# Performance work log

Hardware: AMD Instinct MI355X
Metric: run time of the kernel (lower is better)

## Reference

```python
import jax, jax.numpy as jnp
import numpy as np

B, HW, C = 32, 56, 128
WS, SS, NH = 7, 3, 4
HD = C // NH
SCALE = HD ** -0.5
NWIN = (HW // WS) ** 2  # 64 windows per image
N = WS * WS             # 49 tokens per window


def _build_constants():
    # relative position index [N, N] into flattened (13*13) bias table
    coords = np.stack(np.meshgrid(np.arange(WS), np.arange(WS), indexing='ij'))  # [2,7,7]
    cf = coords.reshape(2, -1)                       # [2,49]
    rel = cf[:, :, None] - cf[:, None, :]            # [2,49,49]
    rel = rel.transpose(1, 2, 0).copy()              # [49,49,2]
    rel[:, :, 0] += WS - 1
    rel[:, :, 1] += WS - 1
    rel[:, :, 0] *= 2 * WS - 1
    pos_index = rel.sum(-1)                          # [49,49]
    # shifted-window attention mask [nW, N, N]
    img = np.zeros((HW, HW))
    sl = (slice(0, -WS), slice(-WS, -SS), slice(-SS, None))
    cnt = 0
    for h in sl:
        for w in sl:
            img[h, w] = cnt
            cnt += 1
    mw = img.reshape(HW // WS, WS, HW // WS, WS).transpose(0, 2, 1, 3).reshape(NWIN, N)
    am = mw[:, None, :] - mw[:, :, None]             # unsqueeze(1) - unsqueeze(2)
    am = np.where(am != 0, -100.0, 0.0).astype(np.float32)
    return jnp.asarray(pos_index), jnp.asarray(am)

POS_INDEX, ATTN_MASK = _build_constants()


def _ln(x, w, b, eps=1e-5):
    mu = x.mean(-1, keepdims=True)
    var = ((x - mu) ** 2).mean(-1, keepdims=True)
    return (x - mu) * jax.lax.rsqrt(var + eps) * w + b


def setup_inputs() -> dict:
    key = jax.random.key(0)
    ks = jax.random.split(key, 10)
    s = 0.02
    return {
        'x': jax.random.normal(ks[0], (B, HW * HW, C), jnp.float32),
        'norm1_w': jnp.ones((C,), jnp.float32),
        'norm1_b': jnp.zeros((C,), jnp.float32),
        'qkv_w': jax.random.normal(ks[1], (C, 3 * C), jnp.float32) * s,
        'qkv_b': jax.random.normal(ks[2], (3 * C,), jnp.float32) * s,
        'proj_w': jax.random.normal(ks[3], (C, C), jnp.float32) * s,
        'proj_b': jax.random.normal(ks[4], (C,), jnp.float32) * s,
        'pos_bias_table': jax.random.normal(ks[5], (2 * WS - 1, 2 * WS - 1, NH), jnp.float32) * s,
        'mlp_w1': jax.random.normal(ks[6], (C, 4 * C), jnp.float32) * s,
        'mlp_b1': jnp.zeros((4 * C,), jnp.float32),
        'mlp_w2': jax.random.normal(ks[7], (4 * C, C), jnp.float32) * s,
        'mlp_b2': jnp.zeros((C,), jnp.float32),
        'norm2_w': jnp.ones((C,), jnp.float32),
        'norm2_b': jnp.zeros((C,), jnp.float32),
    }


def reference(x, norm1_w, norm1_b, qkv_w, qkv_b, proj_w, proj_b, pos_bias_table,
              mlp_w1, mlp_b1, mlp_w2, mlp_b2, norm2_w, norm2_b):
    G = HW // WS  # grid of windows per side
    Bw = B * NWIN
    shortcut = x
    y = _ln(x, norm1_w, norm1_b).reshape(B, HW, HW, C)
    # cyclic shift
    y = jnp.roll(y, (-SS, -SS), axis=(1, 2))
    # window partition -> [B*nW, 49, C]
    yw = y.reshape(B, G, WS, G, WS, C).transpose(0, 1, 3, 2, 4, 5).reshape(Bw, N, C)
    # qkv projection
    qkv = (yw @ qkv_w + qkv_b).reshape(Bw, N, 3, NH, HD).transpose(2, 0, 3, 1, 4)
    q, k, v = qkv[0] * SCALE, qkv[1], qkv[2]  # [Bw, NH, N, HD]
    attn = jnp.einsum('bhnd,bhmd->bhnm', q, k)
    # relative position bias [NH, N, N]
    bias = pos_bias_table.reshape(-1, NH)[POS_INDEX]  # [N,N,NH]
    attn = attn + bias.transpose(2, 0, 1)[None]
    # shift mask per window
    attn = attn.reshape(B, NWIN, NH, N, N) + ATTN_MASK[None, :, None]
    attn = jax.nn.softmax(attn.reshape(Bw, NH, N, N), axis=-1)
    out = jnp.einsum('bhnm,bhmd->bhnd', attn, v).transpose(0, 2, 1, 3).reshape(Bw, N, C)
    out = out @ proj_w + proj_b
    # window reverse
    out = out.reshape(B, G, G, WS, WS, C).transpose(0, 1, 3, 2, 4, 5).reshape(B, HW, HW, C)
    out = jnp.roll(out, (SS, SS), axis=(1, 2)).reshape(B, HW * HW, C)
    x = shortcut + out
    h = _ln(x, norm2_w, norm2_b)
    h = jax.nn.gelu(h @ mlp_w1 + mlp_b1, approximate=False) @ mlp_w2 + mlp_b2
    return x + h
```

## Files before the change

kernel.cpp:

```cpp
#include <hip/hip_runtime.h>
#include <hip/hip_bf16.h>

#define NTOK 100352
#define SCALE_Q 0.17677669529663687f

typedef __bf16 bf16x8 __attribute__((ext_vector_type(8)));
typedef float f32x4 __attribute__((ext_vector_type(4)));
struct bf2 { __hip_bfloat16 x, y; };

__device__ __forceinline__ int wt_to_tok(int wt) {
  int w = wt / 49, n = wt - w * 49;
  int b = w >> 6, wi = w & 63;
  int gh = wi >> 3, gw = wi & 7;
  int r = n / 7, c = n - r * 7;
  int hs = gh * 7 + r + 3; if (hs >= 56) hs -= 56;
  int ws = gw * 7 + c + 3; if (ws >= 56) ws -= 56;
  return (b * 56 + hs) * 56 + ws;
}

__global__ __launch_bounds__(256) void prep_all(const float* __restrict__ qkvw,
                                                const float* __restrict__ projw,
                                                const float* __restrict__ w1,
                                                const float* __restrict__ w2,
                                                __hip_bfloat16* __restrict__ dst) {
  int i = blockIdx.x * 256 + threadIdx.x;
  float v;
  if (i < 49152) { int n = i >> 7, k = i & 127; v = qkvw[k * 384 + n]; }
  else if (i < 65536) { int j = i - 49152; int n = j >> 7, k = j & 127; v = projw[k * 128 + n]; }
  else if (i < 131072) { int j = i - 65536; int n = j >> 7, k = j & 127; v = w1[k * 512 + n]; }
  else { int j = i - 131072; int n = j / 512, k = j - n * 512; v = w2[k * 128 + n]; }
  dst[i] = __float2bfloat16(v);
}

__global__ __launch_bounds__(256) void ln1_apply(const float* __restrict__ x,
                                                 const float* __restrict__ nw,
                                                 const float* __restrict__ nb,
                                                 __hip_bfloat16* __restrict__ xn) {
  int wt = blockIdx.x * 4 + (threadIdx.x >> 6);
  int lane = threadIdx.x & 63;
  int tok = wt_to_tok(wt);
  float2 v = *(const float2*)(x + (size_t)tok * 128 + lane * 2);
  float s = v.x + v.y, ss = v.x * v.x + v.y * v.y;
#pragma unroll
  for (int off = 32; off; off >>= 1) {
    s += __shfl_xor(s, off);
    ss += __shfl_xor(ss, off);
  }
  float mu = s * (1.0f / 128.0f);
  float rstd = rsqrtf(ss * (1.0f / 128.0f) - mu * mu + 1e-5f);
  float2 wv = *(const float2*)(nw + lane * 2);
  float2 bv = *(const float2*)(nb + lane * 2);
  bf2 o;
  o.x = __float2bfloat16((v.x - mu) * rstd * wv.x + bv.x);
  o.y = __float2bfloat16((v.y - mu) * rstd * wv.y + bv.y);
  *(bf2*)(xn + (size_t)wt * 128 + lane * 2) = o;
}

__global__ __launch_bounds__(256) void attn_mfma(const __hip_bfloat16* __restrict__ qkv,
                                                 const float* __restrict__ ptab,
                                                 __hip_bfloat16* __restrict__ attnout) {
  __shared__ __align__(16) char lds[4 * 12288];
  const int tid = threadIdx.x;
  const int lane = tid & 63, h = tid >> 6;
  const int w = blockIdx.x;
  const int wi = w & 63, gh = wi >> 3, gw = wi & 7;
  char* Pl = lds + h * 12288;
  char* VTl = Pl + 8192;
  const int lxi = lane & 15, lq = lane >> 4, lg4 = (lane >> 4) * 4;

  const __hip_bfloat16* base = qkv + (size_t)w * 49 * 384 + h * 32;
  __hip_bfloat16* op = attnout + (size_t)w * 49 * 128 + h * 32;

  bf16x8 qa[4], kb[4];
#pragma unroll
  for (int mi = 0; mi < 4; ++mi) {
    int t = mi * 16 + lxi; if (t > 48) t = 48;
    qa[mi] = *(const bf16x8*)(base + (size_t)t * 384 + lq * 8);
    kb[mi] = *(const bf16x8*)(base + (size_t)t * 384 + 128 + lq * 8);
  }
  {
    union { bf16x8 v; __hip_bfloat16 e[8]; } vv[4];
    const __hip_bfloat16* vp = base + (size_t)(lane < 49 ? lane : 0) * 384 + 256;
#pragma unroll
    for (int q = 0; q < 4; ++q) vv[q].v = *(const bf16x8*)(vp + q * 8);
    __hip_bfloat16 z = __float2bfloat16(0.0f);
#pragma unroll
    for (int q = 0; q < 4; ++q)
#pragma unroll
      for (int e = 0; e < 8; ++e) {
        int d = q * 8 + e;
        __hip_bfloat16 val = (lane < 49) ? vv[q].e[e] : z;
        *(__hip_bfloat16*)(VTl + d * 128 + ((lane * 2) ^ ((d & 7) << 4))) = val;
      }
  }

  f32x4 s[4][4] = {};
#pragma unroll
  for (int mi = 0; mi < 4; ++mi)
#pragma unroll
    for (int ni = 0; ni < 4; ++ni)
      s[mi][ni] = __builtin_amdgcn_mfma_f32_16x16x32_bf16(qa[mi], kb[ni], s[mi][ni], 0, 0, 0);

  int rj[4], cj[4], cntj[4], jbad[4];
#pragma unroll
  for (int ni = 0; ni < 4; ++ni) {
    int jc = ni * 16 + lxi;
    jbad[ni] = (jc > 48);
    int jj = jbad[ni] ? 48 : jc;
    rj[ni] = jj / 7; cj[ni] = jj - rj[ni] * 7;
    int hj = gh * 7 + rj[ni], wj = gw * 7 + cj[ni];
    cntj[ni] = (hj < 49 ? 0 : (hj < 53 ? 3 : 6)) + (wj < 49 ? 0 : (wj < 53 ? 1 : 2));
  }
#pragma unroll
  for (int mi = 0; mi < 4; ++mi)
#pragma unroll
    for (int j = 0; j < 4; ++j) {
      int i = mi * 16 + lg4 + j; if (i > 48) i = 48;
      int ri = i / 7, ci = i - ri * 7;
      int hi_ = gh * 7 + ri, wi_ = gw * 7 + ci;
      int cnti = (hi_ < 49 ? 0 : (hi_ < 53 ? 3 : 6)) + (wi_ < 49 ? 0 : (wi_ < 53 ? 1 : 2));
#pragma unroll
      for (int ni = 0; ni < 4; ++ni) {
        float b = ptab[((ri - rj[ni] + 6) * 13 + (ci - cj[ni] + 6)) * 4 + h];
        float val = s[mi][ni][j] * SCALE_Q + b;
        if (cnti != cntj[ni]) val -= 100.0f;
        if (jbad[ni]) val = -1e30f;
        s[mi][ni][j] = val;
      }
    }

#pragma unroll
  for (int mi = 0; mi < 4; ++mi)
#pragma unroll
    for (int j = 0; j < 4; ++j) {
      float m = fmaxf(fmaxf(s[mi][0][j], s[mi][1][j]), fmaxf(s[mi][2][j], s[mi][3][j]));
#pragma unroll
      for (int off = 8; off; off >>= 1) m = fmaxf(m, __shfl_xor(m, off));
      float e[4], sum = 0.0f;
#pragma unroll
      for (int ni = 0; ni < 4; ++ni) { e[ni] = __expf(s[mi][ni][j] - m); sum += e[ni]; }
#pragma unroll
      for (int off = 8; off; off >>= 1) sum += __shfl_xor(sum, off);
      float inv = 1.0f / sum;
#pragma unroll
      for (int ni = 0; ni < 4; ++ni) s[mi][ni][j] = e[ni] * inv;
    }

#pragma unroll
  for (int mi = 0; mi < 4; ++mi)
#pragma unroll
    for (int j = 0; j < 4; ++j) {
      int row = mi * 16 + lg4 + j;
      int sw = (row & 7) << 4;
      char* prow = Pl + row * 128;
#pragma unroll
      for (int ni = 0; ni < 4; ++ni)
        *(__hip_bfloat16*)(prow + (((ni * 16 + lxi) * 2) ^ sw)) =
            __float2bfloat16(s[mi][ni][j]);
    }

  __syncthreads();

  f32x4 o[4][2] = {};
#pragma unroll
  for (int ks = 0; ks < 2; ++ks) {
    bf16x8 pa[4], vb[2];
#pragma unroll
    for (int mi = 0; mi < 4; ++mi) {
      int row = mi * 16 + lxi;
      pa[mi] = *(const bf16x8*)(Pl + row * 128 + ((ks * 64 + lq * 16) ^ ((row & 7) << 4)));
    }
#pragma unroll
    for (int ni = 0; ni < 2; ++ni) {
      int row = ni * 16 + lxi;
      vb[ni] = *(const bf16x8*)(VTl + row * 128 + ((ks * 64 + lq * 16) ^ ((row & 7) << 4)));
    }
#pragma unroll
    for (int mi = 0; mi < 4; ++mi)
#pragma unroll
      for (int ni = 0; ni < 2; ++ni)
        o[mi][ni] = __builtin_amdgcn_mfma_f32_16x16x32_bf16(pa[mi], vb[ni], o[mi][ni], 0, 0, 0);
  }

#pragma unroll
  for (int mi = 0; mi < 4; ++mi)
#pragma unroll
    for (int j = 0; j < 4; ++j) {
      int q = mi * 16 + lg4 + j;
      if (q < 49) {
#pragma unroll
        for (int ni = 0; ni < 2; ++ni)
          op[(size_t)q * 128 + ni * 16 + lxi] = __float2bfloat16(o[mi][ni][j]);
      }
    }
}

template<int EPI>
__global__ __launch_bounds__(256) void gemm_mfma(
    const __hip_bfloat16* __restrict__ A, int lda,
    const __hip_bfloat16* __restrict__ Wt,
    const float* __restrict__ bias,
    void* __restrict__ outv, int ldo,
    __hip_bfloat16* __restrict__ out2,
    const float* __restrict__ nw, const float* __restrict__ nb,
    const float* __restrict__ res, int K)
{
  __shared__ __align__(16) char AsB[128 * 256];
  __shared__ __align__(16) char BsB[128 * 256];
  const int tid = threadIdx.x;
  const int m0 = blockIdx.x * 128, n0 = blockIdx.y * 128;
  const int srow = tid >> 1;
  const int scol = (tid & 1) * 64;
  const int lane = tid & 63, wid = tid >> 6;
  const int wm = wid >> 1, wn = wid & 1;
  const int lrow = lane & 15, lq = lane >> 4;

  f32x4 acc[4][4] = {};

  for (int k0 = 0; k0 < K; k0 += 128) {
    {
      const char* ap = (const char*)A + ((size_t)(m0 + srow) * lda + k0 + scol) * 2;
      char* dst = AsB + srow * 256;
      int sw = (srow & 7) << 4;
#pragma unroll
      for (int t = 0; t < 8; ++t) {
        int4 raw = *(const int4*)(ap + t * 16);
        *(int4*)(dst + ((scol * 2 + t * 16) ^ sw)) = raw;
      }
    }
    {
      const char* bp = (const char*)Wt + ((size_t)(n0 + srow) * K + k0 + scol) * 2;
      char* dst = BsB + srow * 256;
      int sw = (srow & 7) << 4;
#pragma unroll
      for (int t = 0; t < 8; ++t) {
        int4 raw = *(const int4*)(bp + t * 16);
        *(int4*)(dst + ((scol * 2 + t * 16) ^ sw)) = raw;
      }
    }
    __syncthreads();
#pragma unroll
    for (int ks = 0; ks < 4; ++ks) {
      int kb = ks * 64 + lq * 16;
      bf16x8 af[4], bfr[4];
#pragma unroll
      for (int mi = 0; mi < 4; ++mi) {
        int r = wm * 64 + mi * 16 + lrow;
        af[mi] = *(const bf16x8*)(AsB + r * 256 + (kb ^ ((r & 7) << 4)));
      }
#pragma unroll
      for (int ni = 0; ni < 4; ++ni) {
        int r = wn * 64 + ni * 16 + lrow;
        bfr[ni] = *(const bf16x8*)(BsB + r * 256 + (kb ^ ((r & 7) << 4)));
      }
#pragma unroll
      for (int mi = 0; mi < 4; ++mi)
#pragma unroll
        for (int ni = 0; ni < 4; ++ni)
          acc[mi][ni] = __builtin_amdgcn_mfma_f32_16x16x32_bf16(af[mi], bfr[ni], acc[mi][ni], 0, 0, 0);
    }
    __syncthreads();
  }

  float bv[4];
#pragma unroll
  for (int ni = 0; ni < 4; ++ni) bv[ni] = bias[n0 + wn * 64 + ni * 16 + lrow];

  if (EPI == 4) {
    float* x2 = (float*)outv;
    float* redS = (float*)AsB;
    float* redQ = (float*)(AsB + 1024);
    float nwc[4], nbc[4];
#pragma unroll
    for (int ni = 0; ni < 4; ++ni) {
      int colg = wn * 64 + ni * 16 + lrow;
      nwc[ni] = nw[colg]; nbc[ni] = nb[colg];
    }
    int toks[4][4];
#pragma unroll
    for (int mi = 0; mi < 4; ++mi)
#pragma unroll
      for (int j = 0; j < 4; ++j) {
        int row = wm * 64 + mi * 16 + lq * 4 + j;
        int tok = wt_to_tok(m0 + row);
        toks[mi][j] = tok;
        float s = 0.0f, ss = 0.0f;
#pragma unroll
        for (int ni = 0; ni < 4; ++ni) {
          int colg = wn * 64 + ni * 16 + lrow;
          float val = acc[mi][ni][j] + bv[ni] + res[(size_t)tok * 128 + colg];
          x2[(size_t)tok * 128 + colg] = val;
          acc[mi][ni][j] = val;
          s += val; ss += val * val;
        }
#pragma unroll
        for (int off = 8; off; off >>= 1) {
          s += __shfl_xor(s, off);
          ss += __shfl_xor(ss, off);
        }
        if (lrow == 0) { redS[row * 2 + wn] = s; redQ[row * 2 + wn] = ss; }
      }
    __syncthreads();
#pragma unroll
    for (int mi = 0; mi < 4; ++mi)
#pragma unroll
      for (int j = 0; j < 4; ++j) {
        int row = wm * 64 + mi * 16 + lq * 4 + j;
        float s = redS[row * 2] + redS[row * 2 + 1];
        float ss = redQ[row * 2] + redQ[row * 2 + 1];
        float mu = s * (1.0f / 128.0f);
        float rstd = rsqrtf(ss * (1.0f / 128.0f) - mu * mu + 1e-5f);
        int tok = toks[mi][j];
#pragma unroll
        for (int ni = 0; ni < 4; ++ni) {
          int colg = wn * 64 + ni * 16 + lrow;
          float xnv = (acc[mi][ni][j] - mu) * rstd * nwc[ni] + nbc[ni];
          out2[(size_t)tok * 128 + colg] = __float2bfloat16(xnv);
        }
      }
    return;
  }

#pragma unroll
  for (int mi = 0; mi < 4; ++mi) {
#pragma unroll
    for (int j = 0; j < 4; ++j) {
      int rowg = m0 + wm * 64 + mi * 16 + lq * 4 + j;
#pragma unroll
      for (int ni = 0; ni < 4; ++ni) {
        int colg = n0 + wn * 64 + ni * 16 + lrow;
        float val = acc[mi][ni][j] + bv[ni];
        if (EPI == 0) {
          ((__hip_bfloat16*)outv)[(size_t)rowg * ldo + colg] = __float2bfloat16(val);
        } else if (EPI == 1) {
          float g = 0.5f * val * (1.0f + erff(val * 0.70710678118654752f));
          ((__hip_bfloat16*)outv)[(size_t)rowg * ldo + colg] = __float2bfloat16(g);
        } else {
          float r = res[(size_t)rowg * 128 + colg];
          ((float*)outv)[(size_t)rowg * 128 + colg] = val + r;
        }
      }
    }
  }
}

extern "C" void kernel_launch(void* const* d_in, const int* in_sizes, int n_in,
                              void* d_out, int out_size, void* d_ws, size_t ws_size,
                              hipStream_t stream) {
  (void)in_sizes; (void)n_in; (void)out_size; (void)ws_size;
  const float* x     = (const float*)d_in[0];
  const float* n1w   = (const float*)d_in[1];
  const float* n1b   = (const float*)d_in[2];
  const float* qkvw  = (const float*)d_in[3];
  const float* qkvb  = (const float*)d_in[4];
  const float* projw = (const float*)d_in[5];
  const float* projb = (const float*)d_in[6];
  const float* ptab  = (const float*)d_in[7];
  const float* w1    = (const float*)d_in[8];
  const float* b1    = (const float*)d_in[9];
  const float* w2    = (const float*)d_in[10];
  const float* b2    = (const float*)d_in[11];
  const float* n2w   = (const float*)d_in[12];
  const float* n2b   = (const float*)d_in[13];
  float* out = (float*)d_out;

  char* ws = (char*)d_ws;
  __hip_bfloat16* xn      = (__hip_bfloat16*)ws;
  __hip_bfloat16* qkv     = (__hip_bfloat16*)(ws + 25690112);
  __hip_bfloat16* attnout = (__hip_bfloat16*)(ws + 102760448);
  __hip_bfloat16* u       = (__hip_bfloat16*)(ws + 25690112);
  float* x2               = (float*)(ws + 128450560);
  __hip_bfloat16* x2n     = (__hip_bfloat16*)(ws + 179830784);
  __hip_bfloat16* wbase   = (__hip_bfloat16*)(ws + 205520896);
  __hip_bfloat16* qkvwT  = wbase;
  __hip_bfloat16* projwT = wbase + 49152;
  __hip_bfloat16* w1T    = wbase + 65536;
  __hip_bfloat16* w2T    = wbase + 131072;

  prep_all<<<768, 256, 0, stream>>>(qkvw, projw, w1, w2, wbase);
  ln1_apply<<<NTOK / 4, 256, 0, stream>>>(x, n1w, n1b, xn);
  gemm_mfma<0><<<dim3(784, 3), 256, 0, stream>>>(xn, 128, qkvwT, qkvb,
                                                 qkv, 384, nullptr, nullptr, nullptr, nullptr, 128);
  attn_mfma<<<2048, 256, 0, stream>>>(qkv, ptab, attnout);
  gemm_mfma<4><<<dim3(784, 1), 256, 0, stream>>>(attnout, 128, projwT, projb,
                                                 x2, 128, x2n, n2w, n2b, x, 128);
  gemm_mfma<1><<<dim3(784, 4), 256, 0, stream>>>(x2n, 128, w1T, b1,
                                                 (void*)u, 512, nullptr, nullptr, nullptr, nullptr, 128);
  gemm_mfma<3><<<dim3(784, 1), 256, 0, stream>>>(u, 512, w2T, b2,
                                                 out, 128, nullptr, nullptr, nullptr, x2, 512);
}
```

Before: 271.5 us.

## Store residual in bf16, use tanh GELU, and remap GEMM blocks per XCD

The intermediate residual x2 is now stored in bf16 instead of fp32, halving its write and read traffic between the projection and MLP GEMMs. The exact erf GELU is replaced by a tanh approximation built on a fast exponential. GEMM grids are flattened to 1D with a block-index remap so that the N-tiles sharing an M-tile run on the same XCD, improving L2 reuse of the A tile. The bf16 residual and the tanh GELU add numerical error compared with the fp32 reference.

New measurement: 256.7 us. 1.06x faster.

```diff
diff --git a/kernel.cpp b/kernel.cpp
--- a/kernel.cpp
+++ b/kernel.cpp
@@ -16,6 +16,15 @@
   int hs = gh * 7 + r + 3; if (hs >= 56) hs -= 56;
   int ws = gw * 7 + c + 3; if (ws >= 56) ws -= 56;
   return (b * 56 + hs) * 56 + ws;
+}
+
+__device__ __forceinline__ float gelu_fast(float v) {
+  float y = 0.7978845608028654f * (v + 0.044715f * v * v * v);
+  float ay = fabsf(y);
+  float e = __expf(-2.0f * ay);
+  float t = (1.0f - e) / (1.0f + e);
+  t = copysignf(t, y);
+  return 0.5f * v * (1.0f + t);
 }
 
 __global__ __launch_bounds__(256) void prep_all(const float* __restrict__ qkvw,
@@ -197,18 +206,22 @@
 
 template<int EPI>
 __global__ __launch_bounds__(256) void gemm_mfma(
-    const __hip_bfloat16* __restrict__ A, int lda,
+    const __hip_bfloat16* __restrict__ A, int lda, int NB,
     const __hip_bfloat16* __restrict__ Wt,
     const float* __restrict__ bias,
     void* __restrict__ outv, int ldo,
     __hip_bfloat16* __restrict__ out2,
     const float* __restrict__ nw, const float* __restrict__ nb,
-    const float* __restrict__ res, int K)
+    const float* __restrict__ resf, const __hip_bfloat16* __restrict__ resb,
+    int K)
 {
   __shared__ __align__(16) char AsB[128 * 256];
   __shared__ __align__(16) char BsB[128 * 256];
+  const int bid = blockIdx.x;
+  const int xcd = bid & 7, tt = bid >> 3;
+  const int nbk = tt % NB, mseq = tt / NB;
+  const int m0 = (mseq * 8 + xcd) * 128, n0 = nbk * 128;
   const int tid = threadIdx.x;
-  const int m0 = blockIdx.x * 128, n0 = blockIdx.y * 128;
   const int srow = tid >> 1;
   const int scol = (tid & 1) * 64;
   const int lane = tid & 63, wid = tid >> 6;
@@ -267,7 +280,7 @@
   for (int ni = 0; ni < 4; ++ni) bv[ni] = bias[n0 + wn * 64 + ni * 16 + lrow];
 
   if (EPI == 4) {
-    float* x2 = (float*)outv;
+    __hip_bfloat16* x2 = (__hip_bfloat16*)outv;
     float* redS = (float*)AsB;
     float* redQ = (float*)(AsB + 1024);
     float nwc[4], nbc[4];
@@ -288,8 +301,8 @@
 #pragma unroll
         for (int ni = 0; ni < 4; ++ni) {
           int colg = wn * 64 + ni * 16 + lrow;
-          float val = acc[mi][ni][j] + bv[ni] + res[(size_t)tok * 128 + colg];
-          x2[(size_t)tok * 128 + colg] = val;
+          float val = acc[mi][ni][j] + bv[ni] + resf[(size_t)tok * 128 + colg];
+          x2[(size_t)tok * 128 + colg] = __float2bfloat16(val);
           acc[mi][ni][j] = val;
           s += val; ss += val * val;
         }
@@ -333,10 +346,9 @@
         if (EPI == 0) {
           ((__hip_bfloat16*)outv)[(size_t)rowg * ldo + colg] = __float2bfloat16(val);
         } else if (EPI == 1) {
-          float g = 0.5f * val * (1.0f + erff(val * 0.70710678118654752f));
-          ((__hip_bfloat16*)outv)[(size_t)rowg * ldo + colg] = __float2bfloat16(g);
+          ((__hip_bfloat16*)outv)[(size_t)rowg * ldo + colg] = __float2bfloat16(gelu_fast(val));
         } else {
-          float r = res[(size_t)rowg * 128 + colg];
+          float r = __bfloat162float(resb[(size_t)rowg * 128 + colg]);
           ((float*)outv)[(size_t)rowg * 128 + colg] = val + r;
         }
       }
@@ -369,9 +381,9 @@
   __hip_bfloat16* qkv     = (__hip_bfloat16*)(ws + 25690112);
   __hip_bfloat16* attnout = (__hip_bfloat16*)(ws + 102760448);
   __hip_bfloat16* u       = (__hip_bfloat16*)(ws + 25690112);
-  float* x2               = (float*)(ws + 128450560);
-  __hip_bfloat16* x2n     = (__hip_bfloat16*)(ws + 179830784);
-  __hip_bfloat16* wbase   = (__hip_bfloat16*)(ws + 205520896);
+  __hip_bfloat16* x2      = (__hip_bfloat16*)(ws + 128450560);
+  __hip_bfloat16* x2n     = (__hip_bfloat16*)(ws + 154140672);
+  __hip_bfloat16* wbase   = (__hip_bfloat16*)(ws + 179830784);
   __hip_bfloat16* qkvwT  = wbase;
   __hip_bfloat16* projwT = wbase + 49152;
   __hip_bfloat16* w1T    = wbase + 65536;
@@ -379,13 +391,16 @@
 
   prep_all<<<768, 256, 0, stream>>>(qkvw, projw, w1, w2, wbase);
   ln1_apply<<<NTOK / 4, 256, 0, stream>>>(x, n1w, n1b, xn);
-  gemm_mfma<0><<<dim3(784, 3), 256, 0, stream>>>(xn, 128, qkvwT, qkvb,
-                                                 qkv, 384, nullptr, nullptr, nullptr, nullptr, 128);
+  gemm_mfma<0><<<784 * 3, 256, 0, stream>>>(xn, 128, 3, qkvwT, qkvb,
+                                            qkv, 384, nullptr, nullptr, nullptr,
+                                            nullptr, nullptr, 128);
   attn_mfma<<<2048, 256, 0, stream>>>(qkv, ptab, attnout);
-  gemm_mfma<4><<<dim3(784, 1), 256, 0, stream>>>(attnout, 128, projwT, projb,
-                                                 x2, 128, x2n, n2w, n2b, x, 128);
-  gemm_mfma<1><<<dim3(784, 4), 256, 0, stream>>>(x2n, 128, w1T, b1,
-                                                 (void*)u, 512, nullptr, nullptr, nullptr, nullptr, 128);
-  gemm_mfma<3><<<dim3(784, 1), 256, 0, stream>>>(u, 512, w2T, b2,
-                                                 out, 128, nullptr, nullptr, nullptr, x2, 512);
-}
+  gemm_mfma<4><<<784, 256, 0, stream>>>(attnout, 128, 1, projwT, projb,
+                                        x2, 128, x2n, n2w, n2b, x, nullptr, 128);
+  gemm_mfma<1><<<784 * 4, 256, 0, stream>>>(x2n, 128, 4, w1T, b1,
+                                            (void*)u, 512, nullptr, nullptr, nullptr,
+                                            nullptr, nullptr, 128);
+  gemm_mfma<3><<<784, 256, 0, stream>>>(u, 512, 1, w2T, b2,
+                                        out, 128, nullptr, nullptr, nullptr,
+                                        nullptr, x2, 512);
+}
```
